# Kernel tuning notes

Measured on AMD Instinct MI355X. Metric: run time of the kernel, lower is better.

Reference implementation:

```python
import jax, jax.numpy as jnp
import numpy as np

N_NODES = 10000
N_EDGES = 320000
K = 5
C_IN = 128
C_OUT = 128


def setup_inputs() -> dict:
    key = jax.random.key(0)
    k_h, k_x, k_w, k_b = jax.random.split(key, 4)
    h = jax.random.normal(k_h, (N_NODES, C_IN), dtype=jnp.float32)
    X = jax.random.normal(k_x, (N_EDGES, K), dtype=jnp.float32)
    weight = jax.random.normal(k_w, (K, C_IN, C_OUT), dtype=jnp.float32) * 0.05
    bias = jax.random.normal(k_b, (C_OUT,), dtype=jnp.float32)
    # Unique (src, dst) pairs so scatter-set == segment-sum (matches torch indexing assignment).
    rng = np.random.default_rng(0)
    lin = np.unique(rng.integers(0, N_NODES * N_NODES, size=int(N_EDGES * 1.3)))
    assert len(lin) >= N_EDGES
    lin = lin[:N_EDGES]
    edge_index = jnp.asarray(np.stack([lin // N_NODES, lin % N_NODES]), dtype=jnp.int64)
    batch_node = jnp.zeros((N_NODES,), dtype=jnp.float32)
    return {"h": h, "X": X, "edge_index": edge_index, "batch_node": batch_node,
            "weight": weight, "bias": bias}


def reference(h, X, edge_index, batch_node, weight, bias):
    # Original torch code scatters X.T into a dense (K, N, N) adjacency and does
    # res = A @ h; that equals, per order k:
    #   res[k, i, :] = sum_{e: src_e = i} X[e, k] * h[dst_e, :]
    # which we compute sparsely with segment_sum (edges are unique).
    N = h.shape[0]
    src = edge_index[0]
    dst = edge_index[1]
    h_dst = h[dst]  # [E, C_in] gathered destination features

    def per_k(xk):  # xk: [E] edge values for one order k
        return jax.ops.segment_sum(xk[:, None] * h_dst, src, num_segments=N)  # [N, C_in]

    res_k = jax.vmap(per_k, in_axes=1)(X)  # [K, N, C_in]
    out = jnp.einsum('kni,kio->no', res_k, weight) + bias  # [N, C_out]
    return out
```

## Files before the change

### kernel.cpp

```cpp
#include <hip/hip_runtime.h>

#define N_NODES 10000
#define N_EDGES 320000
#define KDIM 640
#define C_OUT 128

typedef __attribute__((ext_vector_type(8))) short short8;
typedef __attribute__((ext_vector_type(4))) float floatx4;

__device__ __forceinline__ unsigned short f2bf(float f) {
    unsigned int b = __float_as_uint(f);
    b = (b + 0x7FFFu + ((b >> 16) & 1u)) >> 16;
    return (unsigned short)b;
}
__device__ __forceinline__ unsigned int pack2(float x, float y) {
    return (unsigned int)f2bf(x) | ((unsigned int)f2bf(y) << 16);
}
__device__ __forceinline__ float2 unpack2(unsigned int u) {
    float2 r;
    r.x = __uint_as_float(u << 16);
    r.y = __uint_as_float(u & 0xFFFF0000u);
    return r;
}

__global__ __launch_bounds__(256) void prep(
        const float* __restrict__ h, uint2* __restrict__ hb4,
        const float* __restrict__ W, unsigned short* __restrict__ Wt,
        const int* __restrict__ src, int* __restrict__ offsets) {
    const int bid = blockIdx.x;
    const int tid = threadIdx.x;

    if (bid < 1250) {
        const int t = bid * 256 + tid;
        float4 v = ((const float4*)h)[t];
        uint2 o;
        o.x = pack2(v.x, v.y);
        o.y = pack2(v.z, v.w);
        hb4[t] = o;
    } else if (bid < 1330) {
        __shared__ float tile[32][33];
        const int b = bid - 1250;
        const int k0 = (b % 20) * 32, o0 = (b / 20) * 32;
        const int tx = tid & 31, ty = tid >> 5;
#pragma unroll
        for (int i = 0; i < 4; ++i)
            tile[ty + 8 * i][tx] = W[(size_t)(k0 + ty + 8 * i) * C_OUT + o0 + tx];
        __syncthreads();
#pragma unroll
        for (int i = 0; i < 4; ++i)
            Wt[(size_t)(o0 + ty + 8 * i) * KDIM + k0 + tx] = f2bf(tile[tx][ty + 8 * i]);
    } else {
        const int n = (bid - 1330) * 256 + tid;
        if (n > N_NODES) return;
        int lo = 0, hi = N_EDGES;
        while (lo < hi) {
            int mid = (lo + hi) >> 1;
            if (src[mid] < n) lo = mid + 1; else hi = mid;
        }
        offsets[n] = lo;
    }
}

__global__ __launch_bounds__(512, 4) void fused_spectconv(
        const uint2* __restrict__ h4,
        const float* __restrict__ X,
        const int* __restrict__ dst,
        const int* __restrict__ offsets,
        const unsigned short* __restrict__ Wt,
        const float* __restrict__ bias,
        float* __restrict__ out) {
    __shared__ unsigned short Rs[16][648];

    const int tid  = threadIdx.x;
    const int wv   = tid >> 6;
    const int lane = tid & 63;
    const int slot = lane >> 5;
    const int l    = lane & 31;
    const int m0   = blockIdx.x * 16;

    const int node = m0 + wv * 2 + slot;

    float a0x=0,a0y=0,a0z=0,a0w=0, a1x=0,a1y=0,a1z=0,a1w=0,
          a2x=0,a2y=0,a2z=0,a2w=0, a3x=0,a3y=0,a3z=0,a3w=0,
          a4x=0,a4y=0,a4z=0,a4w=0;

    const int e0 = offsets[node];
    const int e1 = offsets[node + 1];

#pragma unroll 4
    for (int e = e0; e < e1; ++e) {
        const int d = dst[e];
        const float x0 = X[(size_t)e * 5 + 0];
        const float x1 = X[(size_t)e * 5 + 1];
        const float x2 = X[(size_t)e * 5 + 2];
        const float x3 = X[(size_t)e * 5 + 3];
        const float x4 = X[(size_t)e * 5 + 4];
        const uint2 u  = h4[(size_t)d * 32 + l];
        const float2 lo = unpack2(u.x), hi = unpack2(u.y);
        a0x = fmaf(x0, lo.x, a0x); a0y = fmaf(x0, lo.y, a0y);
        a0z = fmaf(x0, hi.x, a0z); a0w = fmaf(x0, hi.y, a0w);
        a1x = fmaf(x1, lo.x, a1x); a1y = fmaf(x1, lo.y, a1y);
        a1z = fmaf(x1, hi.x, a1z); a1w = fmaf(x1, hi.y, a1w);
        a2x = fmaf(x2, lo.x, a2x); a2y = fmaf(x2, lo.y, a2y);
        a2z = fmaf(x2, hi.x, a2z); a2w = fmaf(x2, hi.y, a2w);
        a3x = fmaf(x3, lo.x, a3x); a3y = fmaf(x3, lo.y, a3y);
        a3z = fmaf(x3, hi.x, a3z); a3w = fmaf(x3, hi.y, a3w);
        a4x = fmaf(x4, lo.x, a4x); a4y = fmaf(x4, lo.y, a4y);
        a4z = fmaf(x4, hi.x, a4z); a4w = fmaf(x4, hi.y, a4w);
    }

    {
        const int nrel = wv * 2 + slot;
        uint2 w0; w0.x = pack2(a0x, a0y); w0.y = pack2(a0z, a0w);
        uint2 w1; w1.x = pack2(a1x, a1y); w1.y = pack2(a1z, a1w);
        uint2 w2; w2.x = pack2(a2x, a2y); w2.y = pack2(a2z, a2w);
        uint2 w3; w3.x = pack2(a3x, a3y); w3.y = pack2(a3z, a3w);
        uint2 w4; w4.x = pack2(a4x, a4y); w4.y = pack2(a4z, a4w);
        *(uint2*)&Rs[nrel][0 * 128 + 4 * l] = w0;
        *(uint2*)&Rs[nrel][1 * 128 + 4 * l] = w1;
        *(uint2*)&Rs[nrel][2 * 128 + 4 * l] = w2;
        *(uint2*)&Rs[nrel][3 * 128 + 4 * l] = w3;
        *(uint2*)&Rs[nrel][4 * 128 + 4 * l] = w4;
    }

    __syncthreads();

    const int col  = lane & 15;
    const int quad = lane >> 4;
    const int c0   = wv * 16;

    floatx4 acc = {0.f, 0.f, 0.f, 0.f};
    const unsigned short* wrow = Wt + (size_t)(c0 + col) * KDIM + quad * 8;

#pragma unroll
    for (int kc = 0; kc < 20; ++kc) {
        const short8 af = *(const short8*)&Rs[col][kc * 32 + quad * 8];
        const short8 bf = *(const short8*)(wrow + kc * 32);
        acc = __builtin_amdgcn_mfma_f32_16x16x32_bf16(af, bf, acc, 0, 0, 0);
    }

    const float bv = bias[c0 + col];
#pragma unroll
    for (int r = 0; r < 4; ++r) {
        const int m = m0 + quad * 4 + r;
        out[(size_t)m * C_OUT + c0 + col] = acc[r] + bv;
    }
}

extern "C" void kernel_launch(void* const* d_in, const int* in_sizes, int n_in,
                              void* d_out, int out_size, void* d_ws, size_t ws_size,
                              hipStream_t stream) {
    const float* h      = (const float*)d_in[0];
    const float* X      = (const float*)d_in[1];
    const int*   ei     = (const int*)d_in[2];
    const float* weight = (const float*)d_in[4];
    const float* bias   = (const float*)d_in[5];
    float* out = (float*)d_out;

    const int* src = ei;
    const int* dst = ei + N_EDGES;

    char* wsb = (char*)d_ws;
    int*            offsets = (int*)wsb;
    uint2*          hb4     = (uint2*)(wsb + (64 << 10));
    unsigned short* Wtb     = (unsigned short*)(wsb + (64 << 10) + (4 << 20));

    prep<<<1370, 256, 0, stream>>>(h, hb4, weight, Wtb, src, offsets);
    fused_spectconv<<<625, 512, 0, stream>>>(hb4, X, dst, offsets, Wtb, bias, out);
}
```

Baseline: 107.4 us.

## Gather each node with a full wavefront and add nontemporal loads/stores

Each wavefront now processes its two nodes one after another, with all 64 lanes reading 2 bf16 features per edge instead of two half-wavefronts reading 4 each. The edge loop is unrolled by four so the four row gathers are issued before use. The aim is wider coalesced row reads and more loads in flight per wave. Nontemporal hints are also added to the prep loads and the output stores. In exchange, each wave's two nodes are now handled serially, so per-wave latency chains get longer.

```diff
diff --git a/kernel.cpp b/kernel.cpp
--- a/kernel.cpp
+++ b/kernel.cpp
@@ -7,6 +7,7 @@
 
 typedef __attribute__((ext_vector_type(8))) short short8;
 typedef __attribute__((ext_vector_type(4))) float floatx4;
+typedef __attribute__((ext_vector_type(2))) unsigned int uintx2;
 
 __device__ __forceinline__ unsigned short f2bf(float f) {
     unsigned int b = __float_as_uint(f);
@@ -24,7 +25,7 @@
 }
 
 __global__ __launch_bounds__(256) void prep(
-        const float* __restrict__ h, uint2* __restrict__ hb4,
+        const float* __restrict__ h, uintx2* __restrict__ hb4,
         const float* __restrict__ W, unsigned short* __restrict__ Wt,
         const int* __restrict__ src, int* __restrict__ offsets) {
     const int bid = blockIdx.x;
@@ -32,8 +33,8 @@
 
     if (bid < 1250) {
         const int t = bid * 256 + tid;
-        float4 v = ((const float4*)h)[t];
-        uint2 o;
+        floatx4 v = __builtin_nontemporal_load(&((const floatx4*)h)[t]);
+        uintx2 o;
         o.x = pack2(v.x, v.y);
         o.y = pack2(v.z, v.w);
         hb4[t] = o;
@@ -44,7 +45,8 @@
         const int tx = tid & 31, ty = tid >> 5;
 #pragma unroll
         for (int i = 0; i < 4; ++i)
-            tile[ty + 8 * i][tx] = W[(size_t)(k0 + ty + 8 * i) * C_OUT + o0 + tx];
+            tile[ty + 8 * i][tx] =
+                __builtin_nontemporal_load(&W[(size_t)(k0 + ty + 8 * i) * C_OUT + o0 + tx]);
         __syncthreads();
 #pragma unroll
         for (int i = 0; i < 4; ++i)
@@ -62,7 +64,7 @@
 }
 
 __global__ __launch_bounds__(512, 4) void fused_spectconv(
-        const uint2* __restrict__ h4,
+        const unsigned int* __restrict__ h2,
         const float* __restrict__ X,
         const int* __restrict__ dst,
         const int* __restrict__ offsets,
@@ -72,55 +74,59 @@
     __shared__ unsigned short Rs[16][648];
 
     const int tid  = threadIdx.x;
-    const int wv   = tid >> 6;
+    const int wv   = __builtin_amdgcn_readfirstlane(tid >> 6);
     const int lane = tid & 63;
-    const int slot = lane >> 5;
-    const int l    = lane & 31;
     const int m0   = blockIdx.x * 16;
 
-    const int node = m0 + wv * 2 + slot;
+    for (int nn = 0; nn < 2; ++nn) {
+        const int node = m0 + wv * 2 + nn;
+        const int e0 = offsets[node];
+        const int e1 = offsets[node + 1];
 
-    float a0x=0,a0y=0,a0z=0,a0w=0, a1x=0,a1y=0,a1z=0,a1w=0,
-          a2x=0,a2y=0,a2z=0,a2w=0, a3x=0,a3y=0,a3z=0,a3w=0,
-          a4x=0,a4y=0,a4z=0,a4w=0;
+        float a0x=0,a0y=0, a1x=0,a1y=0, a2x=0,a2y=0, a3x=0,a3y=0, a4x=0,a4y=0;
 
-    const int e0 = offsets[node];
-    const int e1 = offsets[node + 1];
+        int e = e0;
+        for (; e + 3 < e1; e += 4) {
+            const int d0 = dst[e + 0];
+            const int d1 = dst[e + 1];
+            const int d2 = dst[e + 2];
+            const int d3 = dst[e + 3];
+            const unsigned int u0 = h2[(size_t)d0 * 64 + lane];
+            const unsigned int u1 = h2[(size_t)d1 * 64 + lane];
+            const unsigned int u2 = h2[(size_t)d2 * 64 + lane];
+            const unsigned int u3 = h2[(size_t)d3 * 64 + lane];
+#pragma unroll
+            for (int q = 0; q < 4; ++q) {
+                const unsigned int u = (q == 0) ? u0 : (q == 1) ? u1 : (q == 2) ? u2 : u3;
+                const float* Xp = X + (size_t)(e + q) * 5;
+                const float x0 = Xp[0], x1 = Xp[1], x2 = Xp[2], x3 = Xp[3], x4 = Xp[4];
+                const float2 hv = unpack2(u);
+                a0x = fmaf(x0, hv.x, a0x); a0y = fmaf(x0, hv.y, a0y);
+                a1x = fmaf(x1, hv.x, a1x); a1y = fmaf(x1, hv.y, a1y);
+                a2x = fmaf(x2, hv.x, a2x); a2y = fmaf(x2, hv.y, a2y);
+                a3x = fmaf(x3, hv.x, a3x); a3y = fmaf(x3, hv.y, a3y);
+                a4x = fmaf(x4, hv.x, a4x); a4y = fmaf(x4, hv.y, a4y);
+            }
+        }
+        for (; e < e1; ++e) {
+            const int d = dst[e];
+            const unsigned int u = h2[(size_t)d * 64 + lane];
+            const float* Xp = X + (size_t)e * 5;
+            const float x0 = Xp[0], x1 = Xp[1], x2 = Xp[2], x3 = Xp[3], x4 = Xp[4];
+            const float2 hv = unpack2(u);
+            a0x = fmaf(x0, hv.x, a0x); a0y = fmaf(x0, hv.y, a0y);
+            a1x = fmaf(x1, hv.x, a1x); a1y = fmaf(x1, hv.y, a1y);
+            a2x = fmaf(x2, hv.x, a2x); a2y = fmaf(x2, hv.y, a2y);
+            a3x = fmaf(x3, hv.x, a3x); a3y = fmaf(x3, hv.y, a3y);
+            a4x = fmaf(x4, hv.x, a4x); a4y = fmaf(x4, hv.y, a4y);
+        }
 
-#pragma unroll 4
-    for (int e = e0; e < e1; ++e) {
-        const int d = dst[e];
-        const float x0 = X[(size_t)e * 5 + 0];
-        const float x1 = X[(size_t)e * 5 + 1];
-        const float x2 = X[(size_t)e * 5 + 2];
-        const float x3 = X[(size_t)e * 5 + 3];
-        const float x4 = X[(size_t)e * 5 + 4];
-        const uint2 u  = h4[(size_t)d * 32 + l];
-        const float2 lo = unpack2(u.x), hi = unpack2(u.y);
-        a0x = fmaf(x0, lo.x, a0x); a0y = fmaf(x0, lo.y, a0y);
-        a0z = fmaf(x0, hi.x, a0z); a0w = fmaf(x0, hi.y, a0w);
-        a1x = fmaf(x1, lo.x, a1x); a1y = fmaf(x1, lo.y, a1y);
-        a1z = fmaf(x1, hi.x, a1z); a1w = fmaf(x1, hi.y, a1w);
-        a2x = fmaf(x2, lo.x, a2x); a2y = fmaf(x2, lo.y, a2y);
-        a2z = fmaf(x2, hi.x, a2z); a2w = fmaf(x2, hi.y, a2w);
-        a3x = fmaf(x3, lo.x, a3x); a3y = fmaf(x3, lo.y, a3y);
-        a3z = fmaf(x3, hi.x, a3z); a3w = fmaf(x3, hi.y, a3w);
-        a4x = fmaf(x4, lo.x, a4x); a4y = fmaf(x4, lo.y, a4y);
-        a4z = fmaf(x4, hi.x, a4z); a4w = fmaf(x4, hi.y, a4w);
-    }
-
-    {
-        const int nrel = wv * 2 + slot;
-        uint2 w0; w0.x = pack2(a0x, a0y); w0.y = pack2(a0z, a0w);
-        uint2 w1; w1.x = pack2(a1x, a1y); w1.y = pack2(a1z, a1w);
-        uint2 w2; w2.x = pack2(a2x, a2y); w2.y = pack2(a2z, a2w);
-        uint2 w3; w3.x = pack2(a3x, a3y); w3.y = pack2(a3z, a3w);
-        uint2 w4; w4.x = pack2(a4x, a4y); w4.y = pack2(a4z, a4w);
-        *(uint2*)&Rs[nrel][0 * 128 + 4 * l] = w0;
-        *(uint2*)&Rs[nrel][1 * 128 + 4 * l] = w1;
-        *(uint2*)&Rs[nrel][2 * 128 + 4 * l] = w2;
-        *(uint2*)&Rs[nrel][3 * 128 + 4 * l] = w3;
-        *(uint2*)&Rs[nrel][4 * 128 + 4 * l] = w4;
+        const int nrel = wv * 2 + nn;
+        *(unsigned int*)&Rs[nrel][0 * 128 + 2 * lane] = pack2(a0x, a0y);
+        *(unsigned int*)&Rs[nrel][1 * 128 + 2 * lane] = pack2(a1x, a1y);
+        *(unsigned int*)&Rs[nrel][2 * 128 + 2 * lane] = pack2(a2x, a2y);
+        *(unsigned int*)&Rs[nrel][3 * 128 + 2 * lane] = pack2(a3x, a3y);
+        *(unsigned int*)&Rs[nrel][4 * 128 + 2 * lane] = pack2(a4x, a4y);
     }
 
     __syncthreads();
@@ -143,7 +149,7 @@
 #pragma unroll
     for (int r = 0; r < 4; ++r) {
         const int m = m0 + quad * 4 + r;
-        out[(size_t)m * C_OUT + c0 + col] = acc[r] + bv;
+        __builtin_nontemporal_store(acc[r] + bv, &out[(size_t)m * C_OUT + c0 + col]);
     }
 }
 
@@ -162,9 +168,10 @@
 
     char* wsb = (char*)d_ws;
     int*            offsets = (int*)wsb;
-    uint2*          hb4     = (uint2*)(wsb + (64 << 10));
+    uintx2*         hb4     = (uintx2*)(wsb + (64 << 10));
     unsigned short* Wtb     = (unsigned short*)(wsb + (64 << 10) + (4 << 20));
 
     prep<<<1370, 256, 0, stream>>>(h, hb4, weight, Wtb, src, offsets);
-    fused_spectconv<<<625, 512, 0, stream>>>(hb4, X, dst, offsets, Wtb, bias, out);
+    fused_spectconv<<<625, 512, 0, stream>>>((const unsigned int*)hb4, X, dst,
+                                             offsets, Wtb, bias, out);
 }
```

Result: no change. 106.0 us (-1.3%).
